# Kernel optimization log

Measured on AMD Instinct MI355X. Metric: run time of the kernel, lower is better.

Reference implementation:

```python
import jax, jax.numpy as jnp
import numpy as np

NODE_DIM = 128
CTX_DIM = 256
OUT_DIM = 256
GRID_SIZE = 4
SPLINE_ORDER = 3
IN_DIM = 3 * NODE_DIM  # subj + obj + transformed context
N_NODES = 100000
N_EDGES = 100000


def make_grid(in_dim, grid_size, spline_order, grid_range=(-1.0, 1.0)):
    h = (grid_range[1] - grid_range[0]) / grid_size
    g = (np.arange(-spline_order, grid_size + spline_order + 1, dtype=np.float32) * h
         + grid_range[0])  # [grid_size + 2*spline_order + 1]
    return jnp.asarray(np.tile(g[None, :], (in_dim, 1)))  # [in, G]


def b_splines(x, grid, spline_order):
    # x: [N, in], grid: [in, G] -> bases: [N, in, grid_size + spline_order]
    xg = x[:, :, None]
    bases = ((xg >= grid[:, :-1]) & (xg < grid[:, 1:])).astype(x.dtype)
    for k in range(1, spline_order + 1):
        left = (xg - grid[:, : -(k + 1)]) / (grid[:, k:-1] - grid[:, : -(k + 1)]) * bases[..., :-1]
        right = (grid[:, k + 1:] - xg) / (grid[:, k + 1:] - grid[:, 1:-k]) * bases[..., 1:]
        bases = left + right
    return bases


def setup_inputs() -> dict:
    key = jax.random.key(0)
    ks = jax.random.split(key, 8)
    n_coef = GRID_SIZE + SPLINE_ORDER
    return {
        "node_embeddings": jax.random.normal(ks[0], (N_NODES, NODE_DIM), jnp.float32),
        "context_embeddings": jax.random.normal(ks[1], (N_EDGES, CTX_DIM), jnp.float32),
        "pair_indices": jax.random.randint(ks[2], (N_EDGES, 2), 0, N_NODES, jnp.int64 if jax.config.jax_enable_x64 else jnp.int32),
        "ctx_w": jax.random.normal(ks[3], (NODE_DIM, CTX_DIM), jnp.float32) * (1.0 / np.sqrt(CTX_DIM)),
        "ctx_b": jnp.zeros((NODE_DIM,), jnp.float32),
        "base_weight": jax.random.normal(ks[4], (OUT_DIM, IN_DIM), jnp.float32) * (1.0 / np.sqrt(IN_DIM)),
        "spline_weight": jax.random.normal(ks[5], (OUT_DIM, IN_DIM, n_coef), jnp.float32) * 0.1,
        "spline_scaler": jax.random.normal(ks[6], (OUT_DIM, IN_DIM), jnp.float32) * (1.0 / np.sqrt(IN_DIM)),
        "grid": make_grid(IN_DIM, GRID_SIZE, SPLINE_ORDER),
    }


def reference(node_embeddings, context_embeddings, pair_indices, ctx_w, ctx_b,
              base_weight, spline_weight, spline_scaler, grid):
    # gather subject/object node embeddings (irregular access)
    subj = node_embeddings[pair_indices[:, 0]]          # [E, node_dim]
    obj = node_embeddings[pair_indices[:, 1]]           # [E, node_dim]
    ctx = context_embeddings @ ctx_w.T + ctx_b          # [E, node_dim]
    x = jnp.concatenate([subj, obj, ctx], axis=1)       # [E, 3*node_dim]

    # efficient-KAN linear layer: base (SiLU) branch + B-spline branch
    base_out = jax.nn.silu(x) @ base_weight.T           # [E, out]
    bsp = b_splines(x, grid, SPLINE_ORDER)              # [E, in, n_coef]
    scaled_w = spline_weight * spline_scaler[:, :, None]  # [out, in, n_coef]
    spline_out = jnp.einsum('nic,oic->no', bsp, scaled_w)
    return base_out + spline_out
```

## Files before the change

kernel.cpp:

```cpp
#include <hip/hip_runtime.h>

#define NEDGES   100000
#define NODE_DIM 128
#define CTX_DIM  256
#define OUT_DIM  256
#define IN_DIM   384
#define NCOEF    7

#define BM2      128
#define BK2      32
#define NCH2     96
#define THR2     512

typedef __bf16 bf16x8 __attribute__((ext_vector_type(8)));
typedef float  f32x4  __attribute__((ext_vector_type(4)));

static __device__ __forceinline__ unsigned short f2bf(float f) {
    unsigned int u = __float_as_uint(f);
    u += 0x7FFFu + ((u >> 16) & 1u);
    return (unsigned short)(u >> 16);
}
static __device__ __forceinline__ float bf2f(unsigned short h) {
    return __uint_as_float(((unsigned int)h) << 16);
}
static __device__ __forceinline__ unsigned int pkbf(float a, float b) {
    unsigned int ua = __float_as_uint(a), ub = __float_as_uint(b);
    ua += 0x7FFFu + ((ua >> 16) & 1u);
    ub += 0x7FFFu + ((ub >> 16) & 1u);
    return (ua >> 16) | (ub & 0xFFFF0000u);
}
static __device__ __forceinline__ float silu(float x) {
    return x / (1.0f + __expf(-x));
}
static __device__ __forceinline__ float n3(float t) {
    float d2 = t - 2.0f;
    float a  = fabsf(d2);
    float p1 = fmaf(fmaf(0.5f, a, -1.0f), d2 * d2, 0.66666667f);
    float dd = fmaxf(2.0f - a, 0.0f);
    float p2 = dd * dd * (dd * (1.0f / 6.0f));
    return a < 1.0f ? p1 : p2;
}

static __device__ __forceinline__ void glds16(const unsigned short* g, unsigned short* l) {
    __builtin_amdgcn_global_load_lds(
        (const __attribute__((address_space(1))) void*)g,
        (__attribute__((address_space(3))) void*)l, 16, 0, 0);
}

__global__ void prep_w2(const float* __restrict__ base_w,
                        const float* __restrict__ spline_w,
                        const float* __restrict__ spline_s,
                        unsigned short* __restrict__ Wsw)
{
    int o = blockIdx.x;
    int i = threadIdx.x;
    int bi = o * IN_DIM + i;
    float sc = spline_s[bi];
    const float* sw = spline_w + (size_t)bi * NCOEF;
    uint4 v;
    v.x = pkbf(base_w[bi], sw[0] * sc);
    v.y = pkbf(sw[1] * sc, sw[2] * sc);
    v.z = pkbf(sw[3] * sc, sw[4] * sc);
    v.w = pkbf(sw[5] * sc, sw[6] * sc);
    int ch = i >> 2, g8 = i & 3;
    int p  = o * 4 + (((o >> 1) + g8) & 3);
    *(uint4*)(Wsw + (size_t)ch * (OUT_DIM * BK2) + p * 8) = v;
}

__global__ void prep_ctxw(const float* __restrict__ ctx_w,
                          unsigned short* __restrict__ B)
{
    int n  = blockIdx.x;
    int k4 = threadIdx.x;
    float4 v = *(const float4*)(ctx_w + (size_t)n * CTX_DIM + k4 * 4);
    *(uint2*)&B[(size_t)n * CTX_DIM + k4 * 4] =
        make_uint2(pkbf(v.x, v.y), pkbf(v.z, v.w));
}

__global__ __launch_bounds__(256)
void gather_x(const float* __restrict__ node_emb,
              const int*   __restrict__ pair,
              unsigned short* __restrict__ Xbf)
{
    const int stride = gridDim.x * blockDim.x;
    const int total  = NEDGES * 64;
    for (int id = blockIdx.x * blockDim.x + threadIdx.x; id < total; id += stride) {
        int f4    = id & 31;
        int which = (id >> 5) & 1;
        int e     = id >> 6;
        int node  = pair[e * 2 + which];
        float4 v = *(const float4*)(node_emb + (size_t)node * NODE_DIM + f4 * 4);
        *(uint2*)&Xbf[(size_t)e * IN_DIM + which * NODE_DIM + f4 * 4] =
            make_uint2(pkbf(v.x, v.y), pkbf(v.z, v.w));
    }
}

#define CG_STR 72
#define CG_ESTR 136
__global__ __launch_bounds__(512, 4)
void ctx_gemm(const float* __restrict__ ctx_emb,
              const unsigned short* __restrict__ ctxwB,
              const float* __restrict__ ctx_b,
              unsigned short* __restrict__ Xbf)
{
    __shared__ unsigned short sm[2 * 128 * CG_STR];
    const int tid    = threadIdx.x;
    const int e_base = blockIdx.x * 128;
    const int wid    = tid >> 6;
    const int lan    = tid & 63;
    const int lrow   = lan & 15;
    const int lquad  = lan >> 4;
    const int m0     = (wid & 1) * 64;
    const int n0     = (wid >> 1) * 32;

    f32x4 acc[4][2];
    #pragma unroll
    for (int a = 0; a < 4; ++a)
        #pragma unroll
        for (int b = 0; b < 2; ++b) { f32x4 z = {0.f,0.f,0.f,0.f}; acc[a][b] = z; }

    #pragma unroll
    for (int it = 0; it < 4; ++it) {
        int id = it * 512 + tid;
        int r  = id >> 4;
        int c4 = id & 15;
        int eg = e_base + r; if (eg >= NEDGES) eg = NEDGES - 1;
        float4 v = *(const float4*)(ctx_emb + (size_t)eg * CTX_DIM + c4 * 4);
        *(uint2*)&sm[r * CG_STR + c4 * 4] = make_uint2(pkbf(v.x, v.y), pkbf(v.z, v.w));
    }
    __syncthreads();

    for (int kc = 0; kc < 4; ++kc) {
        if (kc + 1 < 4) {
            unsigned short* nb = sm + ((kc + 1) & 1) * 128 * CG_STR;
            #pragma unroll
            for (int it = 0; it < 4; ++it) {
                int id = it * 512 + tid;
                int r  = id >> 4;
                int c4 = id & 15;
                int eg = e_base + r; if (eg >= NEDGES) eg = NEDGES - 1;
                float4 v = *(const float4*)(ctx_emb + (size_t)eg * CTX_DIM + (kc + 1) * 64 + c4 * 4);
                *(uint2*)&nb[r * CG_STR + c4 * 4] = make_uint2(pkbf(v.x, v.y), pkbf(v.z, v.w));
            }
        }
        const unsigned short* sa = sm + (kc & 1) * 128 * CG_STR;
        #pragma unroll
        for (int ks = 0; ks < 2; ++ks) {
            int koff = ks * 32 + lquad * 8;
            bf16x8 af[4], bfr[2];
            #pragma unroll
            for (int mt = 0; mt < 4; ++mt)
                af[mt] = *(const bf16x8*)&sa[(m0 + mt*16 + lrow) * CG_STR + koff];
            #pragma unroll
            for (int nt = 0; nt < 2; ++nt)
                bfr[nt] = *(const bf16x8*)&ctxwB[(size_t)(n0 + nt*16 + lrow) * CTX_DIM + kc * 64 + koff];
            #pragma unroll
            for (int mt = 0; mt < 4; ++mt)
                #pragma unroll
                for (int nt = 0; nt < 2; ++nt)
                    acc[mt][nt] = __builtin_amdgcn_mfma_f32_16x16x32_bf16(
                        af[mt], bfr[nt], acc[mt][nt], 0, 0, 0);
        }
        __syncthreads();
    }

    #pragma unroll
    for (int nt = 0; nt < 2; ++nt) {
        int col = n0 + nt * 16 + lrow;
        float cb = ctx_b[col];
        #pragma unroll
        for (int mt = 0; mt < 4; ++mt)
            #pragma unroll
            for (int r = 0; r < 4; ++r) {
                int row = m0 + mt * 16 + lquad * 4 + r;
                sm[row * CG_ESTR + col] = f2bf(acc[mt][nt][r] + cb);
            }
    }
    __syncthreads();
    #pragma unroll
    for (int it = 0; it < 8; ++it) {
        int id  = it * 512 + tid;
        int row = id >> 5;
        int g   = id & 31;
        int eg  = e_base + row; if (eg >= NEDGES) eg = NEDGES - 1;
        *(uint2*)&Xbf[(size_t)eg * IN_DIM + 256 + g * 4] = *(uint2*)&sm[row * CG_ESTR + g * 4];
    }
}

#define A2STR  40
#define A2SZ   (BM2 * A2STR)
#define B2SZ   (OUT_DIM * BK2)
#define OFF_A0 0
#define OFF_A1 A2SZ
#define OFF_B0 (2 * A2SZ)
#define OFF_B1 (2 * A2SZ + B2SZ)
#define LDS2   (2 * A2SZ + 2 * B2SZ)

static __device__ __forceinline__ void gen_elem(
    unsigned short xh, float hinv, float b0, unsigned short* dst)
{
    float x  = bf2f(xh);
    float sl = silu(x);
    unsigned short slh = f2bf(sl);
    float t  = fmaf(x, hinv, b0);
    float jf = floorf(t);
    int   j0 = (int)jf;
    float u  = t - jf;
    float u2 = u * u, u3 = u2 * u;
    float Q0 = u3 * 0.16666667f;
    float d  = 1.0f - u;
    float Q3 = d * d * d * 0.16666667f;
    float Q1 = fmaf(0.5f, u + u2 - u3, 0.16666667f);
    float Q2 = fmaf(0.5f, u3, 0.66666667f - u2);
    unsigned plo = pkbf(Q3, Q2);
    unsigned phi = pkbf(Q1, Q0);
    unsigned long long P = ((unsigned long long)phi << 32) | plo;
    int sh = (j0 << 4) - 32;
    unsigned a  = (unsigned)sh;
    unsigned na = 0u - a;
    unsigned long long lo =
        (a  < 64u) ? (P << (a  & 63u)) : ((na < 64u) ? (P >> (na & 63u)) : 0ull);
    unsigned b2 = a - 64u;
    unsigned nb = 0u - b2;
    unsigned long long hi =
        (b2 < 64u) ? (P << (b2 & 63u)) : ((nb < 64u) ? (P >> (nb & 63u)) : 0ull);
    lo = (lo & ~0xFFFFull) | (unsigned long long)slh;
    uint4 w;
    w.x = (unsigned)lo; w.y = (unsigned)(lo >> 32);
    w.z = (unsigned)hi; w.w = (unsigned)(hi >> 32);
    *(uint4*)dst = w;
}

__global__ __launch_bounds__(THR2, 4)
void kan_gemm2(const unsigned short* __restrict__ Wsw,
               const unsigned short* __restrict__ Xbf,
               const float* __restrict__ grid,
               float* __restrict__ out)
{
    __shared__ unsigned short smem[LDS2];
    const int tid    = threadIdx.x;
    const int e_base = blockIdx.x * BM2;
    const int wid    = tid >> 6;
    const int lan    = tid & 63;
    const int lrow   = lan & 15;
    const int lquad  = lan >> 4;
    const int m0     = (wid & 1) * 64;
    const int n0     = (wid >> 1) * 64;

    const float g0   = grid[0];
    const float hinv = 1.0f / (grid[1] - grid[0]);
    const float b0   = -g0 * hinv;

    const int grow = tid >> 2;
    const int gcol = tid & 3;
    int geg = e_base + grow; if (geg >= NEDGES) geg = NEDGES - 1;
    const unsigned short* xp = Xbf + (size_t)geg * IN_DIM + gcol;
    const unsigned awr = grow * A2STR + gcol * 8;

    f32x4 acc[4][4];
    #pragma unroll
    for (int a = 0; a < 4; ++a)
        #pragma unroll
        for (int b = 0; b < 4; ++b) { f32x4 z = {0.f,0.f,0.f,0.f}; acc[a][b] = z; }

    unsigned short xc = xp[0];
    unsigned short xn = xp[4];

    #pragma unroll
    for (int it = 0; it < 2; ++it) {
        int id = it * THR2 + tid;
        glds16(Wsw + id * 8, &smem[OFF_B0 + id * 8]);
    }
    gen_elem(xc, hinv, b0, &smem[OFF_A0 + awr]);
    __syncthreads();

    for (int kb = 0; kb < NCH2; ++kb) {
        const int cur = kb & 1;
        if (kb + 1 < NCH2) {
            const unsigned short* wc = Wsw + (size_t)(kb + 1) * B2SZ;
            unsigned boff = cur ? OFF_B0 : OFF_B1;
            #pragma unroll
            for (int it = 0; it < 2; ++it) {
                int id = it * THR2 + tid;
                glds16(wc + id * 8, &smem[boff + id * 8]);
            }
            unsigned short xh = xn;
            if (kb + 2 < NCH2) xn = xp[(kb + 2) * 4];
            gen_elem(xh, hinv, b0, &smem[(cur ? OFF_A0 : OFF_A1) + awr]);
        }
        const unsigned ab = cur ? OFF_A1 : OFF_A0;
        const unsigned bb = cur ? OFF_B1 : OFF_B0;
        bf16x8 af[4], bfr[4];
        #pragma unroll
        for (int mt = 0; mt < 4; ++mt)
            af[mt] = *(const bf16x8*)&smem[ab + (m0 + mt*16 + lrow) * A2STR + lquad * 8];
        #pragma unroll
        for (int nt = 0; nt < 4; ++nt) {
            int n = n0 + nt * 16 + lrow;
            bfr[nt] = *(const bf16x8*)&smem[bb + n * 32 + ((((n >> 1) + lquad) & 3) << 3)];
        }
        #pragma unroll
        for (int mt = 0; mt < 4; ++mt)
            #pragma unroll
            for (int nt = 0; nt < 4; ++nt)
                acc[mt][nt] = __builtin_amdgcn_mfma_f32_16x16x32_bf16(
                    af[mt], bfr[nt], acc[mt][nt], 0, 0, 0);
        __syncthreads();
    }

    #pragma unroll
    for (int mt = 0; mt < 4; ++mt) {
        #pragma unroll
        for (int r = 0; r < 4; ++r) {
            int row = m0 + mt * 16 + lquad * 4 + r;
            int eg  = e_base + row;
            if (eg < NEDGES) {
                float* op = out + (size_t)eg * OUT_DIM + n0 + lrow;
                #pragma unroll
                for (int nt = 0; nt < 4; ++nt)
                    op[nt * 16] = acc[mt][nt][r];
            }
        }
    }
}

#define XSTR 392
#define FSTR 72
#define FOFF_X 0
#define FOFF_A (128 * XSTR)
#define FOFF_B (FOFF_A + 128 * FSTR)
#define FLDS (FOFF_B + OUT_DIM * FSTR)

__global__ __launch_bounds__(512, 2)
void fused_fallback(const float* __restrict__ node_emb,
                    const float* __restrict__ ctx_emb,
                    const int*   __restrict__ pair,
                    const float* __restrict__ ctx_w,
                    const float* __restrict__ ctx_b,
                    const float* __restrict__ base_w,
                    const float* __restrict__ spline_w,
                    const float* __restrict__ spline_s,
                    const float* __restrict__ grid,
                    float* __restrict__ out)
{
    __shared__ unsigned short smem[FLDS];
    const int tid    = threadIdx.x;
    const int e_base = blockIdx.x * 128;
    const int wid    = tid >> 6;
    const int lan    = tid & 63;
    const int lrow   = lan & 15;
    const int lquad  = lan >> 4;

    #pragma unroll
    for (int it = 0; it < 16; ++it) {
        int id    = it * 512 + tid;
        int lane4 = id & 31;
        int e     = (id >> 5) & 127;
        int which = id >> 12;
        int eg = e_base + e; if (eg >= NEDGES) eg = NEDGES - 1;
        int node = pair[eg * 2 + which];
        const float4 v = *(const float4*)(node_emb + (size_t)node * NODE_DIM + lane4 * 4);
        *(ushort4*)&smem[FOFF_X + e * XSTR + which * NODE_DIM + lane4 * 4] =
            make_ushort4(f2bf(v.x), f2bf(v.y), f2bf(v.z), f2bf(v.w));
    }
    {
        f32x4 cacc[4][2];
        #pragma unroll
        for (int a = 0; a < 4; ++a)
            #pragma unroll
            for (int b = 0; b < 2; ++b) { f32x4 z = {0.f,0.f,0.f,0.f}; cacc[a][b] = z; }
        const int m0 = (wid & 1) * 64;
        const int n0 = (wid >> 1) * 32;
        for (int kc = 0; kc < 4; ++kc) {
            #pragma unroll
            for (int it = 0; it < 4; ++it) {
                int id = it * 512 + tid;
                int r  = id >> 4;
                int c4 = id & 15;
                int eg = e_base + r; if (eg >= NEDGES) eg = NEDGES - 1;
                float4 v = *(const float4*)(ctx_emb + (size_t)eg * CTX_DIM + kc * 64 + c4 * 4);
                *(ushort4*)&smem[FOFF_A + r * FSTR + c4 * 4] =
                    make_ushort4(f2bf(v.x), f2bf(v.y), f2bf(v.z), f2bf(v.w));
                float4 w = *(const float4*)(ctx_w + (size_t)r * CTX_DIM + kc * 64 + c4 * 4);
                *(ushort4*)&smem[FOFF_B + r * FSTR + c4 * 4] =
                    make_ushort4(f2bf(w.x), f2bf(w.y), f2bf(w.z), f2bf(w.w));
            }
            __syncthreads();
            #pragma unroll
            for (int ks = 0; ks < 2; ++ks) {
                int koff = ks * 32 + lquad * 8;
                bf16x8 af[4], bfr[2];
                #pragma unroll
                for (int mt = 0; mt < 4; ++mt)
                    af[mt] = *(const bf16x8*)&smem[FOFF_A + (m0 + mt*16 + lrow) * FSTR + koff];
                #pragma unroll
                for (int nt = 0; nt < 2; ++nt)
                    bfr[nt] = *(const bf16x8*)&smem[FOFF_B + (n0 + nt*16 + lrow) * FSTR + koff];
                #pragma unroll
                for (int mt = 0; mt < 4; ++mt)
                    #pragma unroll
                    for (int nt = 0; nt < 2; ++nt)
                        cacc[mt][nt] = __builtin_amdgcn_mfma_f32_16x16x32_bf16(
                            af[mt], bfr[nt], cacc[mt][nt], 0, 0, 0);
            }
            __syncthreads();
        }
        #pragma unroll
        for (int mt = 0; mt < 4; ++mt)
            #pragma unroll
            for (int nt = 0; nt < 2; ++nt)
                #pragma unroll
                for (int r = 0; r < 4; ++r) {
                    int row = m0 + mt*16 + lquad*4 + r;
                    int col = n0 + nt*16 + lrow;
                    smem[FOFF_X + row * XSTR + 256 + col] = f2bf(cacc[mt][nt][r] + ctx_b[col]);
                }
    }
    __syncthreads();

    const float g0   = grid[0];
    const float hinv = 1.0f / (grid[1] - grid[0]);

    f32x4 acc[4][4];
    #pragma unroll
    for (int a = 0; a < 4; ++a)
        #pragma unroll
        for (int b = 0; b < 4; ++b) { f32x4 z = {0.f,0.f,0.f,0.f}; acc[a][b] = z; }

    const int m0 = (wid & 1) * 64;
    const int n0 = (wid >> 1) * 64;

    for (int kb = 0; kb < 48; ++kb) {
        const int seg = kb / 6;
        const int i0  = (kb - seg * 6) * 64;
        #pragma unroll
        for (int it = 0; it < 4; ++it) {
            int id = it * 512 + tid;
            int e  = id >> 4;
            int qq = id & 15;
            ushort4 xv = *(const ushort4*)&smem[FOFF_X + e * XSTR + i0 + qq * 4];
            float x0 = bf2f(xv.x), x1 = bf2f(xv.y), x2 = bf2f(xv.z), x3 = bf2f(xv.w);
            unsigned short r0, r1, r2, r3;
            if (seg == 0) {
                r0 = f2bf(silu(x0)); r1 = f2bf(silu(x1));
                r2 = f2bf(silu(x2)); r3 = f2bf(silu(x3));
            } else {
                const float cf = (float)(seg - 1);
                r0 = f2bf(n3((x0 - g0) * hinv - cf));
                r1 = f2bf(n3((x1 - g0) * hinv - cf));
                r2 = f2bf(n3((x2 - g0) * hinv - cf));
                r3 = f2bf(n3((x3 - g0) * hinv - cf));
            }
            *(ushort4*)&smem[FOFF_A + e * FSTR + qq * 4] = make_ushort4(r0, r1, r2, r3);
        }
        #pragma unroll
        for (int it = 0; it < 4; ++it) {
            int id = it * 512 + tid;
            int o  = id >> 4;
            int qq = id & 15;
            unsigned short r0, r1, r2, r3;
            if (seg == 0) {
                const float4 w = *(const float4*)(base_w + (size_t)o * IN_DIM + i0 + qq * 4);
                r0 = f2bf(w.x); r1 = f2bf(w.y); r2 = f2bf(w.z); r3 = f2bf(w.w);
            } else {
                int c  = seg - 1;
                int bi = o * IN_DIM + i0 + qq * 4;
                r0 = f2bf(spline_w[(size_t)(bi    ) * NCOEF + c] * spline_s[bi    ]);
                r1 = f2bf(spline_w[(size_t)(bi + 1) * NCOEF + c] * spline_s[bi + 1]);
                r2 = f2bf(spline_w[(size_t)(bi + 2) * NCOEF + c] * spline_s[bi + 2]);
                r3 = f2bf(spline_w[(size_t)(bi + 3) * NCOEF + c] * spline_s[bi + 3]);
            }
            *(ushort4*)&smem[FOFF_B + o * FSTR + qq * 4] = make_ushort4(r0, r1, r2, r3);
        }
        __syncthreads();
        #pragma unroll
        for (int ks = 0; ks < 2; ++ks) {
            int koff = ks * 32 + lquad * 8;
            bf16x8 af[4], bfr[4];
            #pragma unroll
            for (int mt = 0; mt < 4; ++mt)
                af[mt] = *(const bf16x8*)&smem[FOFF_A + (m0 + mt*16 + lrow) * FSTR + koff];
            #pragma unroll
            for (int nt = 0; nt < 4; ++nt)
                bfr[nt] = *(const bf16x8*)&smem[FOFF_B + (n0 + nt*16 + lrow) * FSTR + koff];
            #pragma unroll
            for (int mt = 0; mt < 4; ++mt)
                #pragma unroll
                for (int nt = 0; nt < 4; ++nt)
                    acc[mt][nt] = __builtin_amdgcn_mfma_f32_16x16x32_bf16(
                        af[mt], bfr[nt], acc[mt][nt], 0, 0, 0);
        }
        __syncthreads();
    }

    #pragma unroll
    for (int mt = 0; mt < 4; ++mt) {
        #pragma unroll
        for (int r = 0; r < 4; ++r) {
            int row = m0 + mt*16 + lquad*4 + r;
            int eg  = e_base + row;
            if (eg < NEDGES) {
                float* op = out + (size_t)eg * OUT_DIM + n0 + lrow;
                #pragma unroll
                for (int nt = 0; nt < 4; ++nt)
                    op[nt * 16] = acc[mt][nt][r];
            }
        }
    }
}

extern "C" void kernel_launch(void* const* d_in, const int* in_sizes, int n_in,
                              void* d_out, int out_size, void* d_ws, size_t ws_size,
                              hipStream_t stream)
{
    const float* node_emb = (const float*)d_in[0];
    const float* ctx_emb  = (const float*)d_in[1];
    const int*   pair     = (const int*)d_in[2];
    const float* ctx_w    = (const float*)d_in[3];
    const float* ctx_b    = (const float*)d_in[4];
    const float* base_w   = (const float*)d_in[5];
    const float* spline_w = (const float*)d_in[6];
    const float* spline_s = (const float*)d_in[7];
    const float* grid     = (const float*)d_in[8];
    float* out = (float*)d_out;

    const int nblk = (NEDGES + BM2 - 1) / BM2;
    const size_t xoff    = 2u * 1024u * 1024u;
    const size_t ctxwoff = 1572864u;
    const size_t need = xoff + (size_t)NEDGES * IN_DIM * sizeof(unsigned short);

    if (ws_size >= need) {
        unsigned short* Wsw   = (unsigned short*)d_ws;
        unsigned short* CtxwB = (unsigned short*)((char*)d_ws + ctxwoff);
        unsigned short* Xbf   = (unsigned short*)((char*)d_ws + xoff);
        prep_w2<<<OUT_DIM, IN_DIM, 0, stream>>>(base_w, spline_w, spline_s, Wsw);
        prep_ctxw<<<128, 64, 0, stream>>>(ctx_w, CtxwB);
        gather_x<<<2048, 256, 0, stream>>>(node_emb, pair, Xbf);
        ctx_gemm<<<nblk, 512, 0, stream>>>(ctx_emb, CtxwB, ctx_b, Xbf);
        kan_gemm2<<<nblk, THR2, 0, stream>>>(Wsw, Xbf, grid, out);
    } else {
        fused_fallback<<<nblk, 512, 0, stream>>>(
            node_emb, ctx_emb, pair, ctx_w, ctx_b, base_w, spline_w, spline_s, grid, out);
    }
}
```

Measured before the change: 453.1 us.

## Fuse node-embedding gather into KAN GEMM and shrink staging buffer to context only

Removes the separate gather_x kernel. The main KAN GEMM now reads subject and object node embeddings directly from node_emb through the pair indices, and ctx_gemm writes only the 128-wide context projection to a smaller bf16 buffer. This saves a launch plus the write and re-read of a 100000x384 bf16 intermediate. In exchange, the GEMM's per-element prefetch does scattered fp32 loads from random node rows with 4-element strides and a branch per chunk, which may coalesce poorly. It also keeps subject/object values at fp32 precision instead of rounding them to bf16 first.

```diff
diff --git a/kernel.cpp b/kernel.cpp
--- a/kernel.cpp
+++ b/kernel.cpp
@@ -77,31 +77,13 @@
         make_uint2(pkbf(v.x, v.y), pkbf(v.z, v.w));
 }
 
-__global__ __launch_bounds__(256)
-void gather_x(const float* __restrict__ node_emb,
-              const int*   __restrict__ pair,
-              unsigned short* __restrict__ Xbf)
-{
-    const int stride = gridDim.x * blockDim.x;
-    const int total  = NEDGES * 64;
-    for (int id = blockIdx.x * blockDim.x + threadIdx.x; id < total; id += stride) {
-        int f4    = id & 31;
-        int which = (id >> 5) & 1;
-        int e     = id >> 6;
-        int node  = pair[e * 2 + which];
-        float4 v = *(const float4*)(node_emb + (size_t)node * NODE_DIM + f4 * 4);
-        *(uint2*)&Xbf[(size_t)e * IN_DIM + which * NODE_DIM + f4 * 4] =
-            make_uint2(pkbf(v.x, v.y), pkbf(v.z, v.w));
-    }
-}
-
 #define CG_STR 72
 #define CG_ESTR 136
 __global__ __launch_bounds__(512, 4)
 void ctx_gemm(const float* __restrict__ ctx_emb,
               const unsigned short* __restrict__ ctxwB,
               const float* __restrict__ ctx_b,
-              unsigned short* __restrict__ Xbf)
+              unsigned short* __restrict__ CtxB)
 {
     __shared__ unsigned short sm[2 * 128 * CG_STR];
     const int tid    = threadIdx.x;
@@ -183,7 +165,7 @@
         int row = id >> 5;
         int g   = id & 31;
         int eg  = e_base + row; if (eg >= NEDGES) eg = NEDGES - 1;
-        *(uint2*)&Xbf[(size_t)eg * IN_DIM + 256 + g * 4] = *(uint2*)&sm[row * CG_ESTR + g * 4];
+        *(uint2*)&CtxB[(size_t)eg * 128 + g * 4] = *(uint2*)&sm[row * CG_ESTR + g * 4];
     }
 }
 
@@ -197,9 +179,8 @@
 #define LDS2   (2 * A2SZ + 2 * B2SZ)
 
 static __device__ __forceinline__ void gen_elem(
-    unsigned short xh, float hinv, float b0, unsigned short* dst)
-{
-    float x  = bf2f(xh);
+    float x, float hinv, float b0, unsigned short* dst)
+{
     float sl = silu(x);
     unsigned short slh = f2bf(sl);
     float t  = fmaf(x, hinv, b0);
@@ -231,9 +212,19 @@
     *(uint4*)dst = w;
 }
 
+static __device__ __forceinline__ float fetchx(
+    const float* ps, const float* po, const unsigned short* pc, int ch)
+{
+    if (ch < 32) return ps[ch << 2];
+    if (ch < 64) return po[(ch - 32) << 2];
+    return bf2f(pc[(ch - 64) << 2]);
+}
+
 __global__ __launch_bounds__(THR2, 4)
 void kan_gemm2(const unsigned short* __restrict__ Wsw,
-               const unsigned short* __restrict__ Xbf,
+               const unsigned short* __restrict__ CtxB,
+               const float* __restrict__ node_emb,
+               const int*   __restrict__ pair,
                const float* __restrict__ grid,
                float* __restrict__ out)
 {
@@ -254,7 +245,11 @@
     const int grow = tid >> 2;
     const int gcol = tid & 3;
     int geg = e_base + grow; if (geg >= NEDGES) geg = NEDGES - 1;
-    const unsigned short* xp = Xbf + (size_t)geg * IN_DIM + gcol;
+    const int nsub = pair[geg * 2 + 0];
+    const int nobj = pair[geg * 2 + 1];
+    const float* ps = node_emb + (size_t)nsub * NODE_DIM + gcol;
+    const float* po = node_emb + (size_t)nobj * NODE_DIM + gcol;
+    const unsigned short* pc = CtxB + (size_t)geg * 128 + gcol;
     const unsigned awr = grow * A2STR + gcol * 8;
 
     f32x4 acc[4][4];
@@ -263,8 +258,8 @@
         #pragma unroll
         for (int b = 0; b < 4; ++b) { f32x4 z = {0.f,0.f,0.f,0.f}; acc[a][b] = z; }
 
-    unsigned short xc = xp[0];
-    unsigned short xn = xp[4];
+    float xc = fetchx(ps, po, pc, 0);
+    float xn = fetchx(ps, po, pc, 1);
 
     #pragma unroll
     for (int it = 0; it < 2; ++it) {
@@ -284,8 +279,8 @@
                 int id = it * THR2 + tid;
                 glds16(wc + id * 8, &smem[boff + id * 8]);
             }
-            unsigned short xh = xn;
-            if (kb + 2 < NCH2) xn = xp[(kb + 2) * 4];
+            float xh = xn;
+            if (kb + 2 < NCH2) xn = fetchx(ps, po, pc, kb + 2);
             gen_elem(xh, hinv, b0, &smem[(cur ? OFF_A0 : OFF_A1) + awr]);
         }
         const unsigned ab = cur ? OFF_A1 : OFF_A0;
@@ -525,19 +520,18 @@
     float* out = (float*)d_out;
 
     const int nblk = (NEDGES + BM2 - 1) / BM2;
+    const size_t ctxwoff = 1572864u;
     const size_t xoff    = 2u * 1024u * 1024u;
-    const size_t ctxwoff = 1572864u;
-    const size_t need = xoff + (size_t)NEDGES * IN_DIM * sizeof(unsigned short);
+    const size_t need = xoff + (size_t)NEDGES * 128 * sizeof(unsigned short);
 
     if (ws_size >= need) {
         unsigned short* Wsw   = (unsigned short*)d_ws;
         unsigned short* CtxwB = (unsigned short*)((char*)d_ws + ctxwoff);
-        unsigned short* Xbf   = (unsigned short*)((char*)d_ws + xoff);
+        unsigned short* CtxB  = (unsigned short*)((char*)d_ws + xoff);
         prep_w2<<<OUT_DIM, IN_DIM, 0, stream>>>(base_w, spline_w, spline_s, Wsw);
         prep_ctxw<<<128, 64, 0, stream>>>(ctx_w, CtxwB);
-        gather_x<<<2048, 256, 0, stream>>>(node_emb, pair, Xbf);
-        ctx_gemm<<<nblk, 512, 0, stream>>>(ctx_emb, CtxwB, ctx_b, Xbf);
-        kan_gemm2<<<nblk, THR2, 0, stream>>>(Wsw, Xbf, grid, out);
+        ctx_gemm<<<nblk, 512, 0, stream>>>(ctx_emb, CtxwB, ctx_b, CtxB);
+        kan_gemm2<<<nblk, THR2, 0, stream>>>(Wsw, CtxB, node_emb, pair, grid, out);
     } else {
         fused_fallback<<<nblk, 512, 0, stream>>>(
             node_emb, ctx_emb, pair, ctx_w, ctx_b, base_w, spline_w, spline_s, grid, out);
```

Measured after the change: 446.1 us. No clear change (-1.5%).
